# Kernel tuning notes

Hardware: AMD Instinct MI355X
Metric: run time of the kernel (lower is better)

Reference implementation:

```python
import jax, jax.numpy as jnp
import numpy as np

NUM_ORI = 4
VM_R, VM_RG = 10.0, 15.0
B_INH, G_INH = 1.5, 1.0
VM_W, VM_W2 = 0.1, 0.4
VM_WG, VM_W2G = 0.2, 0.4
BORDER_K = 11   # int(10*1.1)=11, already odd
GROUP_K = 23    # int(15*1.5)=22 -> +1 to make odd


def create_von_mises(size, r0, theta0, centered, w, w2):
    x = np.arange(size) - size / 2
    y = -(np.arange(size) - size / 2)
    X, Y = np.meshgrid(x, y)
    if centered:
        X = X + r0 * np.cos(theta0)
        Y = Y + r0 * np.sin(theta0)
    r = np.sqrt(X ** 2 + Y ** 2)
    th = np.arctan2(Y, X)
    # np.i0 == scipy.special.iv(0, .) for real args (I0 is even)
    return np.exp(r0 * w * np.cos(th - theta0)) / np.i0(w2 * (r - r0))


def make_filters():
    borders, groups = [], []
    for ori in np.arange(0.0, 180.0, 180.0 / NUM_ORI):
        a = ori * np.pi / 180.0
        b = (ori + 180.0) * np.pi / 180.0
        borders.append(create_von_mises(BORDER_K, VM_R, a, True, VM_W, VM_W2))
        borders.append(create_von_mises(BORDER_K, VM_R, b, True, VM_W, VM_W2))
        g1 = create_von_mises(GROUP_K, VM_RG, a, False, VM_W, VM_W2)
        g2 = create_von_mises(GROUP_K, VM_RG, b, False, VM_WG, VM_W2G)
        groups += [g1, g1, g2, g2]
    # only border filters are normalized to [-1, 1] in the original code
    borders = [f / (f.max() / 2.0) - 1.0 for f in borders]
    Wb = np.stack(borders)[:, None].astype(np.float32)   # [2*O, 1, 11, 11]
    Wg = np.stack(groups)[:, None].astype(np.float32)    # [4*O, 1, 23, 23]
    return jnp.asarray(Wb), jnp.asarray(Wg)


def setup_inputs() -> dict:
    key = jax.random.key(0)
    inp = jax.random.uniform(key, (4, 2, 512, 512), dtype=jnp.float32)
    Wb, Wg = make_filters()
    return {"inp": inp, "W_border": Wb, "W_group": Wg}


def _conv(x, w, pad, groups):
    return jax.lax.conv_general_dilated(
        x, w, (1, 1), [(pad, pad), (pad, pad)],
        dimension_numbers=("NCHW", "OIHW", "NCHW"),
        feature_group_count=groups)


def _spike(v):
    # LIF with tau_mem=0.01, zero initial v_mem, single step: alpha=exp(-1/tau)~0,
    # so v_mem = input; spike when v_mem >= threshold (1.0).
    return (v >= 1.0).astype(v.dtype)


def reference(inp, W_border, W_group):
    B, _, H, W = inp.shape
    pad_b = (BORDER_K - 1) // 2
    pad_g = (GROUP_K - 1) // 2
    # border ownership: conv each polarity with the 8 von-Mises filters + LIF
    pos = _spike(_conv(inp[:, 0:1], W_border, pad_b, 1))  # [B, 2*O, H, W]
    neg = _spike(_conv(inp[:, 1:2], W_border, pad_b, 1))
    vmap_ = inp.sum(1)[:, None]                           # [B, 1, H, W]
    pe, po = pos[:, 0::2], pos[:, 1::2]   # even=ori, odd=opposite ori
    ne, no = neg[:, 0::2], neg[:, 1::2]
    b13 = _spike(vmap_ * (pe - no * B_INH)) + _spike(vmap_ * (ne - po * B_INH))
    b24 = _spike(vmap_ * (po - ne * B_INH)) + _spike(vmap_ * (no - pe * B_INH))
    # winner-take-all over orientations
    diff = b13 - b24                                      # [B, O, H, W]
    tp = jnp.abs(diff)
    wta = jax.lax.stop_gradient(
        (tp == tp.max(axis=1, keepdims=True)).astype(inp.dtype))
    b1p = _spike(wta * diff)
    b1n = _spike(-(wta * diff))
    # channel order is ori-major: [t1_o, t2_o, t3_o, t4_o] per orientation
    border = jnp.stack(
        [b1p * b13, b1p * b24 * G_INH, b1n * b24, b1n * b13 * G_INH],
        axis=2).reshape(B, 4 * NUM_ORI, H, W)
    g = _spike(_conv(border, W_group, pad_g, 4 * NUM_ORI))
    g = g.reshape(B, NUM_ORI, 4, H, W)
    return (_spike(g[:, :, 0] - g[:, :, 1])
            + _spike(g[:, :, 2] - g[:, :, 3])).sum(1)     # [B, H, W]
```

## Files before the change

kernel.cpp:

```cpp
#include <hip/hip_runtime.h>

#define HH 512
#define WW 512
#define NB 4

#define K1 11
#define PAD1 5
#define T1X 32
#define T1Y 16
#define IN1X 42
#define IN1Y 26
#define S1 44

__device__ __forceinline__ unsigned conv8_pass2(const float* __restrict__ sm,
                                                const float* __restrict__ Wb,
                                                int py, int px)
{
    float acc[8][2];
    #pragma unroll
    for (int c = 0; c < 8; c++) { acc[c][0] = 0.f; acc[c][1] = 0.f; }

    #pragma unroll 1
    for (int ky = 0; ky < K1; ky++) {
        const float2* rp = (const float2*)&sm[(py + ky) * S1 + px];
        float a[12];
        #pragma unroll
        for (int r = 0; r < 6; r++) *(float2*)&a[2 * r] = rp[r];
        #pragma unroll
        for (int c = 0; c < 8; c++) {
            #pragma unroll
            for (int kx = 0; kx < K1; kx++) {
                const float wv = Wb[c * 121 + ky * 11 + kx];
                acc[c][0] = fmaf(a[kx],     wv, acc[c][0]);
                acc[c][1] = fmaf(a[kx + 1], wv, acc[c][1]);
            }
        }
    }
    unsigned bits = 0;
    #pragma unroll
    for (int c = 0; c < 8; c++) {
        bits |= (acc[c][0] >= 1.f ? 1u : 0u) << (c * 2);
        bits |= (acc[c][1] >= 1.f ? 1u : 0u) << (c * 2 + 1);
    }
    return bits;
}

__global__ __launch_bounds__(256, 8) void stage1_kernel(
    const float* __restrict__ inp, const float* __restrict__ Wb,
    unsigned char* __restrict__ border)
{
    __shared__ __align__(16) float s0[IN1Y * S1];
    __shared__ __align__(16) float s1[IN1Y * S1];

    const int b   = blockIdx.z;
    const int tx0 = blockIdx.x * T1X;
    const int ty0 = blockIdx.y * T1Y;
    const float* in0 = inp + ((size_t)b * 2 + 0) * (HH * WW);
    const float* in1 = inp + ((size_t)b * 2 + 1) * (HH * WW);

    for (int i = threadIdx.x; i < IN1Y * IN1X; i += 256) {
        int iy = i / IN1X, ix = i - iy * IN1X;
        int gy = ty0 + iy - PAD1, gx = tx0 + ix - PAD1;
        bool ok = (gy >= 0) & (gy < HH) & (gx >= 0) & (gx < WW);
        int idx = gy * WW + gx;
        s0[iy * S1 + ix] = ok ? in0[idx] : 0.f;
        s1[iy * S1 + ix] = ok ? in1[idx] : 0.f;
    }
    __syncthreads();

    const int lx = threadIdx.x & 15;
    const int ly = threadIdx.x >> 4;
    const int px = lx * 2;
    const int py = ly;

    const unsigned bitP = conv8_pass2(s0, Wb, py, px);
    const unsigned bitN = conv8_pass2(s1, Wb, py, px);

    const int gy = ty0 + py;
    const int gxbase = tx0 + px;

    float vm[2];
    #pragma unroll
    for (int p = 0; p < 2; p++)
        vm[p] = s0[(py + PAD1) * S1 + px + PAD1 + p]
              + s1[(py + PAD1) * S1 + px + PAD1 + p];

    float b13[4][2], b24[4][2];
    #pragma unroll
    for (int o = 0; o < 4; o++) {
        #pragma unroll
        for (int p = 0; p < 2; p++) {
            float pe = (float)((bitP >> (4 * o + p))     & 1u);
            float po = (float)((bitP >> (4 * o + 2 + p)) & 1u);
            float ne = (float)((bitN >> (4 * o + p))     & 1u);
            float no = (float)((bitN >> (4 * o + 2 + p)) & 1u);
            float sa = (vm[p] * (pe - 1.5f * no) >= 1.f) ? 1.f : 0.f;
            float sb = (vm[p] * (ne - 1.5f * po) >= 1.f) ? 1.f : 0.f;
            b13[o][p] = sa + sb;
            float sc = (vm[p] * (po - 1.5f * ne) >= 1.f) ? 1.f : 0.f;
            float sd = (vm[p] * (no - 1.5f * pe) >= 1.f) ? 1.f : 0.f;
            b24[o][p] = sc + sd;
        }
    }
    float mxp[2];
    #pragma unroll
    for (int p = 0; p < 2; p++) {
        float m = 0.f;
        #pragma unroll
        for (int o = 0; o < 4; o++) m = fmaxf(m, fabsf(b13[o][p] - b24[o][p]));
        mxp[p] = m;
    }
    #pragma unroll
    for (int o = 0; o < 4; o++) {
        unsigned short w0 = 0, w1 = 0, w2 = 0, w3 = 0;
        #pragma unroll
        for (int p = 0; p < 2; p++) {
            float d   = b13[o][p] - b24[o][p];
            float wta = (fabsf(d) == mxp[p]) ? 1.f : 0.f;
            float b1p = (wta * d >= 1.f)    ? 1.f : 0.f;
            float b1n = (-(wta * d) >= 1.f) ? 1.f : 0.f;
            w0 |= (unsigned short)(unsigned char)(b1p * b13[o][p]) << (8 * p);
            w1 |= (unsigned short)(unsigned char)(b1p * b24[o][p]) << (8 * p);
            w2 |= (unsigned short)(unsigned char)(b1n * b24[o][p]) << (8 * p);
            w3 |= (unsigned short)(unsigned char)(b1n * b13[o][p]) << (8 * p);
        }
        size_t base = (((size_t)b * 16 + 4 * o) * HH + gy) * WW + gxbase;
        *(unsigned short*)&border[base]                       = w0;
        *(unsigned short*)&border[base + (size_t)HH * WW]     = w1;
        *(unsigned short*)&border[base + (size_t)2 * HH * WW] = w2;
        *(unsigned short*)&border[base + (size_t)3 * HH * WW] = w3;
    }
}

#define K2 23
#define PAD2 11
#define T2X 32
#define T2Y 512
#define SROW 18
#define R2 534

__device__ __forceinline__ float ubyte_f(unsigned dw, int byi) {
    return (float)((dw >> (8 * byi)) & 0xffu);
}

__device__ __forceinline__ void s2_row(const unsigned* __restrict__ tile,
                                       int trow, int lx, float a[31])
{
    unsigned d[8];
    const uint2* tp2 = (const uint2*)&tile[trow * SROW + 2 * lx];
    #pragma unroll
    for (int r2 = 0; r2 < 4; r2++) {
        uint2 v = tp2[r2];
        d[2 * r2] = v.x; d[2 * r2 + 1] = v.y;
    }
    #pragma unroll
    for (int j = 1; j <= 30; j++) a[j] = ubyte_f(d[j >> 2], j & 3);
}

__global__ __launch_bounds__(256, 4) void stage2_kernel(
    const unsigned char* __restrict__ border, const float* __restrict__ Wg,
    unsigned char* __restrict__ gsp)
{
    __shared__ unsigned tile[R2 * SROW];

    const int z   = blockIdx.z;
    const int b   = z >> 4;
    const int c   = z & 15;
    const int tx0 = blockIdx.x * T2X;
    const unsigned char* bp = border + ((size_t)b * 16 + c) * (HH * WW);

    for (int i = threadIdx.x; i < R2 * 16; i += 256) {
        int iy = i >> 4, cc = i & 15;
        int gy  = iy - PAD2;
        int gx0 = tx0 - 12 + 4 * cc;
        unsigned u = 0;
        if (((unsigned)gy < HH) & ((unsigned)gx0 < WW))
            u = *(const unsigned*)(bp + (size_t)gy * WW + gx0);
        tile[iy * SROW + cc] = u;
    }
    __syncthreads();

    const int lx = threadIdx.x & 3;
    const int ly = threadIdx.x >> 2;
    const int px = lx * 8;
    const int py = ly * 8;

    float acc[8][8];
    #pragma unroll
    for (int dy = 0; dy < 8; dy++)
        #pragma unroll
        for (int p = 0; p < 8; p++) acc[dy][p] = 0.f;

    const float* wc = Wg + c * (K2 * K2);

    #pragma unroll 1
    for (int t = 0; t < 7; t++) {
        float a[31];
        s2_row(tile, py + t, lx, a);
        #pragma unroll
        for (int dy = 0; dy < 8; dy++) {
            if (t - dy >= 0) {
                const float* wr = wc + (t - dy) * K2;
                #pragma unroll
                for (int kx = 0; kx < K2; kx++) {
                    const float wv = wr[kx];
                    #pragma unroll
                    for (int p = 0; p < 8; p++)
                        acc[dy][p] = fmaf(a[p + kx + 1], wv, acc[dy][p]);
                }
            }
        }
    }

    #pragma unroll 1
    for (int t = 7; t < 23; t++) {
        float a[31];
        s2_row(tile, py + t, lx, a);
        const float* w0 = wc + t * K2;
        #pragma unroll
        for (int kx = 0; kx < K2; kx++) {
            float wv[8];
            #pragma unroll
            for (int d = 0; d < 8; d++) wv[d] = w0[kx - 23 * d];
            #pragma unroll
            for (int p = 0; p < 8; p++) {
                const float av = a[p + kx + 1];
                #pragma unroll
                for (int d = 0; d < 8; d++)
                    acc[d][p] = fmaf(av, wv[d], acc[d][p]);
            }
        }
    }

    #pragma unroll 1
    for (int t = 23; t < 30; t++) {
        float a[31];
        s2_row(tile, py + t, lx, a);
        #pragma unroll
        for (int dy = 0; dy < 8; dy++) {
            if (t - dy < K2) {
                const float* wr = wc + (t - dy) * K2;
                #pragma unroll
                for (int kx = 0; kx < K2; kx++) {
                    const float wv = wr[kx];
                    #pragma unroll
                    for (int p = 0; p < 8; p++)
                        acc[dy][p] = fmaf(a[p + kx + 1], wv, acc[dy][p]);
                }
            }
        }
    }

    const int ox = tx0 + px;
    unsigned char* gp = gsp + ((size_t)b * 16 + c) * (HH * WW);
    #pragma unroll
    for (int dy = 0; dy < 8; dy++) {
        const int oy = py + dy;
        unsigned lo = 0, hi = 0;
        #pragma unroll
        for (int p = 0; p < 4; p++) lo |= (acc[dy][p]     >= 1.f ? 1u : 0u) << (8 * p);
        #pragma unroll
        for (int p = 0; p < 4; p++) hi |= (acc[dy][p + 4] >= 1.f ? 1u : 0u) << (8 * p);
        uint2 v; v.x = lo; v.y = hi;
        *(uint2*)&gp[(size_t)oy * WW + ox] = v;
    }
}

__global__ __launch_bounds__(256) void combine_kernel(
    const unsigned char* __restrict__ gsp, float* __restrict__ out)
{
    const int idx = blockIdx.x * 256 + threadIdx.x;
    const int b = idx >> 16;
    const int r = idx & 65535;
    const unsigned* g = (const unsigned*)gsp;
    const int pb = b * 16;
    unsigned s = 0;
    #pragma unroll
    for (int o = 0; o < 4; o++) {
        unsigned g0 = g[(size_t)(pb + 4 * o + 0) * 65536 + r];
        unsigned g1 = g[(size_t)(pb + 4 * o + 1) * 65536 + r];
        unsigned g2 = g[(size_t)(pb + 4 * o + 2) * 65536 + r];
        unsigned g3 = g[(size_t)(pb + 4 * o + 3) * 65536 + r];
        s += ((g0 & ~g1) & 0x01010101u) + ((g2 & ~g3) & 0x01010101u);
    }
    float4 f;
    f.x = (float)(s & 255u);
    f.y = (float)((s >> 8) & 255u);
    f.z = (float)((s >> 16) & 255u);
    f.w = (float)(s >> 24);
    ((float4*)out)[idx] = f;
}

extern "C" void kernel_launch(void* const* d_in, const int* in_sizes, int n_in,
                              void* d_out, int out_size, void* d_ws, size_t ws_size,
                              hipStream_t stream)
{
    const float* inp = (const float*)d_in[0];
    const float* Wb  = (const float*)d_in[1];
    const float* Wg  = (const float*)d_in[2];
    unsigned char* border = (unsigned char*)d_ws;
    unsigned char* gsp    = border + (size_t)NB * 16 * HH * WW;
    float* out = (float*)d_out;

    dim3 blk(256);
    dim3 g1(WW / T1X, HH / T1Y, NB);
    stage1_kernel<<<g1, blk, 0, stream>>>(inp, Wb, border);
    dim3 g2(WW / T2X, 1, NB * 16);
    stage2_kernel<<<g2, blk, 0, stream>>>(border, Wg, gsp);
    dim3 g3((NB * HH * WW / 4) / 256);
    combine_kernel<<<g3, blk, 0, stream>>>(gsp, out);
}
```

Before: 272.4 us.

## Prepack conv weights into d-contiguous layout and prefetch next tile row

```diff
diff --git a/kernel.cpp b/kernel.cpp
--- a/kernel.cpp
+++ b/kernel.cpp
@@ -3,6 +3,32 @@
 #define HH 512
 #define WW 512
 #define NB 4
+
+#define WG2_ELEMS 47104
+#define WB2_ELEMS 968
+
+__global__ __launch_bounds__(256) void prep_kernel(
+    const float* __restrict__ Wb, const float* __restrict__ Wg,
+    float* __restrict__ wscr)
+{
+    const int e = blockIdx.x * 256 + threadIdx.x;
+    if (e < WG2_ELEMS) {
+        const int d  = e & 7;
+        const int r  = e >> 3;
+        const int kx = r % 23;
+        const int r2 = r / 23;
+        const int tt = r2 & 15;
+        const int c  = r2 >> 4;
+        wscr[e] = Wg[c * 529 + (tt + 7 - d) * 23 + kx];
+    } else if (e < WG2_ELEMS + WB2_ELEMS) {
+        const int f  = e - WG2_ELEMS;
+        const int ky = f / 88;
+        const int q  = f - ky * 88;
+        const int c  = q / 11;
+        const int kx = q - c * 11;
+        wscr[e] = Wb[c * 121 + ky * 11 + kx];
+    }
+}
 
 #define K1 11
 #define PAD1 5
@@ -13,7 +39,7 @@
 #define S1 44
 
 __device__ __forceinline__ unsigned conv8_pass2(const float* __restrict__ sm,
-                                                const float* __restrict__ Wb,
+                                                const float* __restrict__ Wb2,
                                                 int py, int px)
 {
     float acc[8][2];
@@ -26,11 +52,12 @@
         float a[12];
         #pragma unroll
         for (int r = 0; r < 6; r++) *(float2*)&a[2 * r] = rp[r];
+        const float* wr = Wb2 + ky * 88;
         #pragma unroll
         for (int c = 0; c < 8; c++) {
             #pragma unroll
             for (int kx = 0; kx < K1; kx++) {
-                const float wv = Wb[c * 121 + ky * 11 + kx];
+                const float wv = wr[c * 11 + kx];
                 acc[c][0] = fmaf(a[kx],     wv, acc[c][0]);
                 acc[c][1] = fmaf(a[kx + 1], wv, acc[c][1]);
             }
@@ -46,7 +73,7 @@
 }
 
 __global__ __launch_bounds__(256, 8) void stage1_kernel(
-    const float* __restrict__ inp, const float* __restrict__ Wb,
+    const float* __restrict__ inp, const float* __restrict__ Wb2,
     unsigned char* __restrict__ border)
 {
     __shared__ __align__(16) float s0[IN1Y * S1];
@@ -73,8 +100,8 @@
     const int px = lx * 2;
     const int py = ly;
 
-    const unsigned bitP = conv8_pass2(s0, Wb, py, px);
-    const unsigned bitN = conv8_pass2(s1, Wb, py, px);
+    const unsigned bitP = conv8_pass2(s0, Wb2, py, px);
+    const unsigned bitN = conv8_pass2(s1, Wb2, py, px);
 
     const int gy = ty0 + py;
     const int gxbase = tx0 + px;
@@ -139,27 +166,40 @@
 #define SROW 18
 #define R2 534
 
+typedef const float __attribute__((address_space(1)))* gfp;
+
+__device__ __forceinline__ gfp as_global_vec(const float* p) {
+    asm volatile("" : "+v"(p));
+    return (gfp)(unsigned long long)p;
+}
+
 __device__ __forceinline__ float ubyte_f(unsigned dw, int byi) {
     return (float)((dw >> (8 * byi)) & 0xffu);
 }
 
-__device__ __forceinline__ void s2_row(const unsigned* __restrict__ tile,
-                                       int trow, int lx, float a[31])
-{
-    unsigned d[8];
+__device__ __forceinline__ void s2_load(const unsigned* __restrict__ tile,
+                                        int trow, int lx, unsigned d[8])
+{
     const uint2* tp2 = (const uint2*)&tile[trow * SROW + 2 * lx];
     #pragma unroll
     for (int r2 = 0; r2 < 4; r2++) {
         uint2 v = tp2[r2];
         d[2 * r2] = v.x; d[2 * r2 + 1] = v.y;
     }
+}
+
+__device__ __forceinline__ void s2_row(const unsigned* __restrict__ tile,
+                                       int trow, int lx, float a[31])
+{
+    unsigned d[8];
+    s2_load(tile, trow, lx, d);
     #pragma unroll
     for (int j = 1; j <= 30; j++) a[j] = ubyte_f(d[j >> 2], j & 3);
 }
 
 __global__ __launch_bounds__(256, 4) void stage2_kernel(
     const unsigned char* __restrict__ border, const float* __restrict__ Wg,
-    unsigned char* __restrict__ gsp)
+    const float* __restrict__ Wg2, unsigned char* __restrict__ gsp)
 {
     __shared__ unsigned tile[R2 * SROW];
 
@@ -212,16 +252,21 @@
         }
     }
 
+    const gfp wbase = as_global_vec(Wg2 + (size_t)c * 16 * 184);
+    unsigned dc[8];
+    s2_load(tile, py + 7, lx, dc);
     #pragma unroll 1
     for (int t = 7; t < 23; t++) {
         float a[31];
-        s2_row(tile, py + t, lx, a);
-        const float* w0 = wc + t * K2;
+        #pragma unroll
+        for (int j = 1; j <= 30; j++) a[j] = ubyte_f(dc[j >> 2], j & 3);
+        s2_load(tile, py + t + 1, lx, dc);
+        const gfp wt = wbase + (t - 7) * 184;
         #pragma unroll
         for (int kx = 0; kx < K2; kx++) {
             float wv[8];
             #pragma unroll
-            for (int d = 0; d < 8; d++) wv[d] = w0[kx - 23 * d];
+            for (int d = 0; d < 8; d++) wv[d] = wt[kx * 8 + d];
             #pragma unroll
             for (int p = 0; p < 8; p++) {
                 const float av = a[p + kx + 1];
@@ -302,11 +347,16 @@
     unsigned char* gsp    = border + (size_t)NB * 16 * HH * WW;
     float* out = (float*)d_out;
 
+    float* wscr = (float*)((char*)d_out + (2u << 20));
+    const float* Wg2 = wscr;
+    const float* Wb2 = wscr + WG2_ELEMS;
+
     dim3 blk(256);
+    prep_kernel<<<dim3((WG2_ELEMS + WB2_ELEMS + 255) / 256), blk, 0, stream>>>(Wb, Wg, wscr);
     dim3 g1(WW / T1X, HH / T1Y, NB);
-    stage1_kernel<<<g1, blk, 0, stream>>>(inp, Wb, border);
+    stage1_kernel<<<g1, blk, 0, stream>>>(inp, Wb2, border);
     dim3 g2(WW / T2X, 1, NB * 16);
-    stage2_kernel<<<g2, blk, 0, stream>>>(border, Wg, gsp);
+    stage2_kernel<<<g2, blk, 0, stream>>>(border, Wg, Wg2, gsp);
     dim3 g3((NB * HH * WW / 4) / 256);
     combine_kernel<<<g3, blk, 0, stream>>>(gsp, out);
 }
```

Measured after the change: 294.6 us. +8.1%, slower.
